# Kernel tuning notes

Measured on AMD Instinct MI355X. Metric: run time of the kernel, lower is better.

The kernel has to match this reference:

```python
import jax, jax.numpy as jnp
import numpy as np

N, E, F_IN, H, NSE, L, C, G = 50000, 800000, 128, 128, 16, 3, 10, 256


def setup_inputs() -> dict:
    key = jax.random.key(0)
    ks = jax.random.split(key, 32)
    sc = 0.05
    inp = {
        "x": jax.random.normal(ks[0], (N, F_IN), jnp.float32),
        "s": jax.random.normal(ks[1], (N, NSE), jnp.float32),
        "edge_index": jax.random.randint(ks[2], (2, E), 0, N, jnp.int64),
        "batch": jnp.sort(jax.random.randint(ks[3], (N,), 0, G, jnp.int64)),
        # pre: Linear(F_IN, H); embedding_s: Linear(NSE, H)
        "pre_w": jax.random.normal(ks[4], (F_IN, H), jnp.float32) * sc,
        "pre_b": jnp.zeros((H,), jnp.float32),
        "emb_w": jax.random.normal(ks[5], (NSE, H), jnp.float32) * sc,
        "emb_b": jnp.zeros((H,), jnp.float32),
        # per-layer GIN MLP: Linear(2H,H) -> ReLU -> Linear(H,H)
        "gin_w1": jax.random.normal(ks[6], (L, 2 * H, H), jnp.float32) * sc,
        "gin_b1": jnp.zeros((L, H), jnp.float32),
        "gin_w2": jax.random.normal(ks[7], (L, H, H), jnp.float32) * sc,
        "gin_b2": jnp.zeros((L, H), jnp.float32),
        # per-layer GCNConv(H, H)
        "gcn_w": jax.random.normal(ks[8], (L, H, H), jnp.float32) * sc,
        "gcn_b": jnp.zeros((L, H), jnp.float32),
        "whp_w": jax.random.normal(ks[9], (2 * H, H), jnp.float32) * sc,
        "whp_b": jnp.zeros((H,), jnp.float32),
        "post_w": jax.random.normal(ks[10], (H, H), jnp.float32) * sc,
        "post_b": jnp.zeros((H,), jnp.float32),
        "ro_w": jax.random.normal(ks[11], (H, C), jnp.float32) * sc,
        "ro_b": jnp.zeros((C,), jnp.float32),
    }
    return inp


def reference(x, s, edge_index, batch, pre_w, pre_b, emb_w, emb_b,
              gin_w1, gin_b1, gin_w2, gin_b2, gcn_w, gcn_b,
              whp_w, whp_b, post_w, post_b, ro_w, ro_b):
    src, dst = edge_index[0], edge_index[1]
    x = x @ pre_w + pre_b                      # [N, H]
    s = s @ emb_w + emb_b                      # [N, H]
    # GCN symmetric norm with self-loops (deg includes the +1 self loop)
    deg = jax.ops.segment_sum(jnp.ones((E,), x.dtype), dst, num_segments=N) + 1.0
    dinv = jax.lax.rsqrt(deg)                  # [N]
    enorm = (dinv[src] * dinv[dst])[:, None]   # [E, 1]
    self_norm = (dinv * dinv)[:, None]         # [N, 1]
    for i in range(L):
        xc = jnp.concatenate([x, s], axis=-1)  # [N, 2H]
        # GINConv (eps=0): nn(x_i + sum_j x_j)
        agg = jax.ops.segment_sum(xc[src], dst, num_segments=N)
        h = xc + agg
        h = jax.nn.relu(h @ gin_w1[i] + gin_b1[i]) @ gin_w2[i] + gin_b2[i]
        x = jax.nn.relu(h)                     # dropout is identity in eval mode
        # GCNConv on s stream
        hs = s @ gcn_w[i]
        sagg = jax.ops.segment_sum(hs[src] * enorm, dst, num_segments=N)
        s = jnp.tanh(sagg + hs * self_norm + gcn_b[i])
    x = jnp.concatenate([x, s], axis=-1) @ whp_w + whp_b
    g = jax.ops.segment_sum(x, batch, num_segments=G)   # global_add_pool [G, H]
    g = jax.nn.relu(g @ post_w + post_b)
    return jax.nn.log_softmax(g @ ro_w + ro_b, axis=1)
```

## Files before the change

### kernel.cpp

```cpp
#include <hip/hip_runtime.h>
#include <math.h>

typedef __attribute__((ext_vector_type(8))) short short8;
typedef __attribute__((ext_vector_type(4))) float f32x4;
typedef unsigned int uint;
typedef unsigned short ushort;

#define HGRID(n, b) (((n) + (b) - 1) / (b))

__device__ __forceinline__ ushort f2bu(float f) {
    uint x = __builtin_bit_cast(uint, f);
    x = (x + 0x7fffu + ((x >> 16) & 1u)) >> 16;
    return (ushort)x;
}
__device__ __forceinline__ float blo(uint u) {
    return __builtin_bit_cast(float, u << 16);
}
__device__ __forceinline__ float bhi(uint u) {
    return __builtin_bit_cast(float, u & 0xffff0000u);
}
__device__ __forceinline__ uint packbf(float a, float b) {
    return (uint)f2bu(a) | ((uint)f2bu(b) << 16);
}

__device__ __forceinline__ void gload16(const void* g, void* l) {
    __builtin_amdgcn_global_load_lds(
        (const __attribute__((address_space(1))) void*)g,
        (__attribute__((address_space(3))) void*)l, 16, 0, 0);
}


__global__ void init_kernel(int* __restrict__ cnt, int* __restrict__ cur,
                            float* __restrict__ gbuf, int N, int GH) {
    int i = blockIdx.x * 256 + threadIdx.x;
    if (i < N) { cnt[i] = 0; cur[i] = 0; }
    if (i < GH) gbuf[i] = 0.f;
}


__global__ void count_kernel(const int* __restrict__ dst, int* __restrict__ cnt, int E) {
    int e = blockIdx.x * 256 + threadIdx.x;
    if (e < E) atomicAdd(&cnt[dst[e]], 1);
}

__global__ void scan_part(const int* __restrict__ cnt, int* __restrict__ bsum, int N) {
    __shared__ int sh[256];
    int b = blockIdx.x, t = threadIdx.x;
    int base = b * 1024 + t * 4;
    int tsum = 0;
    if (base + 3 < N) {
        int4 v = *(const int4*)(cnt + base);
        tsum = v.x + v.y + v.z + v.w;
    } else {
        #pragma unroll
        for (int k = 0; k < 4; ++k) if (base + k < N) tsum += cnt[base + k];
    }
    sh[t] = tsum;
    __syncthreads();
    for (int d = 128; d > 0; d >>= 1) {
        if (t < d) sh[t] += sh[t + d];
        __syncthreads();
    }
    if (t == 0) bsum[b] = sh[0];
}

__global__ void scan_fill(const int* __restrict__ cnt, const int* __restrict__ bsum,
                          int* __restrict__ offs, float* __restrict__ dinv,
                          int N, int E) {
    __shared__ int sh[256];
    __shared__ int sbase;
    int b = blockIdx.x, t = threadIdx.x;

    if (t < 64) {
        int s = 0;
        for (int i = t; i < b; i += 64) s += bsum[i];
        #pragma unroll
        for (int d = 32; d > 0; d >>= 1) s += __shfl_down(s, d, 64);
        if (t == 0) sbase = s;
    }

    int base = b * 1024 + t * 4;
    int c[4] = {0, 0, 0, 0};
    if (base + 3 < N) {
        int4 v = *(const int4*)(cnt + base);
        c[0] = v.x; c[1] = v.y; c[2] = v.z; c[3] = v.w;
    } else {
        #pragma unroll
        for (int k = 0; k < 4; ++k) if (base + k < N) c[k] = cnt[base + k];
    }
    int tsum = c[0] + c[1] + c[2] + c[3];
    sh[t] = tsum;
    __syncthreads();
    for (int d = 1; d < 256; d <<= 1) {
        int o = (t >= d) ? sh[t - d] : 0;
        __syncthreads();
        sh[t] += o;
        __syncthreads();
    }
    int run = sbase + sh[t] - tsum;
    #pragma unroll
    for (int k = 0; k < 4; ++k) {
        if (base + k < N) {
            offs[base + k] = run;
            dinv[base + k] = rsqrtf((float)c[k] + 1.0f);
            run += c[k];
        }
    }
    if (b == 0 && t == 0) offs[N] = E;
}

__global__ void fill_kernel(const int* __restrict__ src, const int* __restrict__ dst,
                            const int* __restrict__ offs, int* __restrict__ cur,
                            const float* __restrict__ dinv, int2* __restrict__ epack, int E) {
    int e = blockIdx.x * 256 + threadIdx.x;
    if (e < E) {
        int d = dst[e];
        int sv = src[e];
        int p = offs[d] + atomicAdd(&cur[d], 1);
        epack[p] = make_int2(sv * 64, __float_as_int(dinv[sv]));
    }
}


struct PrepArgs {
    const float *x, *s;
    const float *pre_w, *pre_b, *emb_w, *emb_b, *gin_w1, *gcn_w, *gin_w2, *whp_w;
    ushort *xs, *Wt_preemb, *Wt_dual, *Wt_gin2, *Wt_whp;
    float *bias_comb;
    int L, N;
};

__global__ void prep_kernel(PrepArgs a) {
    long idx = (long)blockIdx.x * 256 + threadIdx.x;
    long nconv = (long)a.N * 24;
    if (idx < nconv) {
        int n = (int)(idx / 24), ch = (int)(idx % 24);
        uint4 o = {0u, 0u, 0u, 0u};
        if (ch < 16) {
            const float4* px = (const float4*)(a.x + (long)n * 128 + ch * 8);
            float4 u = px[0], v = px[1];
            o.x = packbf(u.x, u.y); o.y = packbf(u.z, u.w);
            o.z = packbf(v.x, v.y); o.w = packbf(v.z, v.w);
        } else if (ch < 18) {
            const float4* ps = (const float4*)(a.s + (long)n * 16 + (ch - 16) * 8);
            float4 u = ps[0], v = ps[1];
            o.x = packbf(u.x, u.y); o.y = packbf(u.z, u.w);
            o.z = packbf(v.x, v.y); o.w = packbf(v.z, v.w);
        }
        *(uint4*)(a.xs + idx * 8) = o;
        return;
    }
    idx -= nconv;
    if (idx < 49152) {
        int c = (int)(idx / 192), k = (int)(idx % 192);
        float v = 0.f;
        if (c < 128) { if (k < 128) v = a.pre_w[(long)k * 128 + c]; }
        else if (k >= 128 && k < 144) v = a.emb_w[(long)(k - 128) * 128 + (c - 128)];
        a.Wt_preemb[idx] = f2bu(v);
        return;
    }
    idx -= 49152;
    if (idx < (long)a.L * 65536) {
        int i = (int)(idx / 65536);
        int r = (int)(idx % 65536);
        int c = r / 256, k = r % 256;
        float v = 0.f;
        if (c < 128) v = a.gin_w1[(long)i * 32768 + (long)k * 128 + c];
        else if (k >= 128) v = a.gcn_w[(long)i * 16384 + (long)(k - 128) * 128 + (c - 128)];
        a.Wt_dual[idx] = f2bu(v);
        return;
    }
    idx -= (long)a.L * 65536;
    if (idx < (long)a.L * 16384) {
        int i = (int)(idx / 16384);
        int r = (int)(idx % 16384);
        int c = r / 128, k = r % 128;
        a.Wt_gin2[idx] = f2bu(a.gin_w2[(long)i * 16384 + (long)k * 128 + c]);
        return;
    }
    idx -= (long)a.L * 16384;
    if (idx < 32768) {
        int c = (int)(idx / 256), k = (int)(idx % 256);
        a.Wt_whp[idx] = f2bu(a.whp_w[(long)k * 128 + c]);
        return;
    }
    idx -= 32768;
    if (idx < 256) a.bias_comb[idx] = (idx < 128) ? a.pre_b[idx] : a.emb_b[idx - 128];
}


template<int KPAD, int BN>
__global__ __launch_bounds__(512) void lin_mfma(
    const ushort* __restrict__ A, int a_stride,
    const ushort* __restrict__ Wt, const float* __restrict__ bias,
    ushort* __restrict__ out, int o_stride, int N, int act, int interleaved)
{
    constexpr int BK = 64;
    constexpr int NF = BN / 64;
    __shared__ __align__(16) ushort LA[128][BK];
    __shared__ __align__(16) ushort LB[BN][BK];

    const int tid  = threadIdx.x;
    const int l    = tid & 63;
    const int w    = tid >> 6;
    const int wr   = w >> 2;
    const int wc   = w & 3;
    const int row0 = blockIdx.x * 128;
    const int l15  = l & 15;
    const int lhi  = l >> 4;
    const int lrow = l >> 3;
    const int lslot = l & 7;

    f32x4 acc[4][NF];
    #pragma unroll
    for (int m = 0; m < 4; ++m)
        #pragma unroll
        for (int n = 0; n < NF; ++n) acc[m][n] = (f32x4){0.f, 0.f, 0.f, 0.f};

    for (int k0 = 0; k0 < KPAD; k0 += BK) {
        __syncthreads();
        #pragma unroll
        for (int i = 0; i < 2; ++i) {
            int ci = w * 2 + i;
            int r  = ci * 8 + lrow;
            int gr = row0 + r; if (gr > N - 1) gr = N - 1;
            gload16(A + (long)gr * a_stride + k0 + ((lslot ^ (r & 7)) * 8), &LA[ci * 8][0]);
        }
        #pragma unroll
        for (int i = 0; i < NF; ++i) {
            int ci = w * NF + i;
            int c  = ci * 8 + lrow;
            gload16(Wt + (long)c * KPAD + k0 + ((lslot ^ (c & 7)) * 8), &LB[ci * 8][0]);
        }
        __syncthreads();
        #pragma unroll
        for (int kk = 0; kk < BK; kk += 32) {
            int chb = (kk >> 3) + lhi;
            short8 a[4];
            #pragma unroll
            for (int m = 0; m < 4; ++m) {
                int r = wr * 64 + m * 16 + l15;
                a[m] = *(const short8*)&LA[r][(chb ^ (r & 7)) * 8];
            }
            #pragma unroll
            for (int n = 0; n < NF; ++n) {
                int c = wc * (BN / 4) + n * 16 + l15;
                short8 b = *(const short8*)&LB[c][(chb ^ (c & 7)) * 8];
                #pragma unroll
                for (int m = 0; m < 4; ++m)
                    acc[m][n] = __builtin_amdgcn_mfma_f32_16x16x32_bf16(a[m], b, acc[m][n], 0, 0, 0);
            }
        }
    }

    #pragma unroll
    for (int n = 0; n < NF; ++n) {
        int col = wc * (BN / 4) + n * 16 + l15;
        float bv = bias ? bias[col] : 0.f;
        #pragma unroll
        for (int m = 0; m < 4; ++m) {
            #pragma unroll
            for (int j = 0; j < 4; ++j) {
                int gr = row0 + wr * 64 + m * 16 + (lhi << 2) + j;
                if (gr < N) {
                    float v = acc[m][n][j] + bv;
                    if (act) v = fmaxf(v, 0.f);
                    long off;
                    if (interleaved) {
                        int cc = col & 127;
                        off = (long)gr * 256 + 4 * (cc >> 1) + ((col >> 7) << 1) + (cc & 1);
                    } else {
                        off = (long)gr * o_stride + col;
                    }
                    out[off] = f2bu(v);
                }
            }
        }
    }
}


__global__ __launch_bounds__(256) void fused_gather(
    const uint2* __restrict__ yh, const int* __restrict__ offs,
    const int2* __restrict__ epack,
    const float* __restrict__ dinv,
    const float* __restrict__ b1, const float* __restrict__ gb,
    uint* __restrict__ h1p, uint* __restrict__ xcp, int N)
{
    int node = blockIdx.x * 4 + (threadIdx.x >> 6);
    if (node >= N) return;
    int l = threadIdx.x & 63;

    uint2 self = yh[(long)node * 64 + l];
    float di = dinv[node];
    float g0 = blo(self.x), g1 = bhi(self.x);
    float s0 = 0.f, s1 = 0.f;

    int j0 = offs[node], j1 = offs[node + 1];
    int jmid = j0 + ((j1 - j0) & ~7);

    for (int j = j0; j < jmid; j += 8) {
        int2 e[8]; uint2 v[8];
        #pragma unroll
        for (int k = 0; k < 8; ++k) e[k] = epack[j + k];
        #pragma unroll
        for (int k = 0; k < 8; ++k) v[k] = yh[e[k].x + l];
        #pragma unroll
        for (int k = 0; k < 8; ++k) {
            float ds = __int_as_float(e[k].y);
            g0 += blo(v[k].x);
            g1 += bhi(v[k].x);
            s0 += blo(v[k].y) * ds;
            s1 += bhi(v[k].y) * ds;
        }
    }
    if (jmid < j1) {
        int2 e[8]; uint2 v[8];
        #pragma unroll
        for (int k = 0; k < 8; ++k) {
            int jj = jmid + k;
            e[k] = epack[(jj < j1) ? jj : (j1 - 1)];
            if (jj >= j1) e[k].y = 0;
        }
        #pragma unroll
        for (int k = 0; k < 8; ++k) v[k] = yh[e[k].x + l];
        #pragma unroll
        for (int k = 0; k < 8; ++k) {
            float ds = __int_as_float(e[k].y);
            float m = (jmid + k < j1) ? 1.f : 0.f;
            g0 += blo(v[k].x) * m;
            g1 += bhi(v[k].x) * m;
            s0 += blo(v[k].y) * ds;
            s1 += bhi(v[k].y) * ds;
        }
    }

    float2 bb = ((const float2*)b1)[l];
    g0 = fmaxf(g0 + bb.x, 0.f);
    g1 = fmaxf(g1 + bb.y, 0.f);
    h1p[(long)node * 64 + l] = packbf(g0, g1);

    float dii = di * di;
    float2 gg = ((const float2*)gb)[l];
    float t0 = tanhf(s0 * di + blo(self.y) * dii + gg.x);
    float t1 = tanhf(s1 * di + bhi(self.y) * dii + gg.y);
    xcp[(long)node * 128 + 64 + l] = packbf(t0, t1);
}


__global__ void pool_kernel(const ushort* __restrict__ xh, const int* __restrict__ batch,
                            float* __restrict__ g, int N) {
    int c  = threadIdx.x;
    int n0 = blockIdx.x * 128;
    if (n0 >= N) return;
    int n1 = min(n0 + 128, N);
    int curg = batch[n0];
    float acc = 0.f;
    for (int n = n0; n < n1; ++n) {
        int b = batch[n];
        if (b != curg) {
            atomicAdd(&g[(long)curg * 128 + c], acc);
            acc = 0.f;
            curg = b;
        }
        acc += blo((uint)xh[(long)n * 128 + c]);
    }
    atomicAdd(&g[(long)curg * 128 + c], acc);
}


__global__ void head_kernel(const float* __restrict__ g, const float* __restrict__ post_w,
                            const float* __restrict__ post_b, const float* __restrict__ ro_w,
                            const float* __restrict__ ro_b, float* __restrict__ out, int C) {
    __shared__ float row[128];
    __shared__ float g2[128];
    __shared__ float lg[16];
    __shared__ float s_lse;
    int gi = blockIdx.x;
    int c  = threadIdx.x;
    row[c] = g[(long)gi * 128 + c];
    __syncthreads();
    float acc = post_b[c];
    for (int k = 0; k < 128; ++k) acc += row[k] * post_w[k * 128 + c];
    g2[c] = fmaxf(acc, 0.f);
    __syncthreads();
    if (c < C) {
        float a = ro_b[c];
        for (int k = 0; k < 128; ++k) a += g2[k] * ro_w[k * C + c];
        lg[c] = a;
    }
    __syncthreads();
    if (c == 0) {
        float m = lg[0];
        for (int i = 1; i < C; ++i) m = fmaxf(m, lg[i]);
        float sum = 0.f;
        for (int i = 0; i < C; ++i) sum += expf(lg[i] - m);
        s_lse = m + logf(sum);
    }
    __syncthreads();
    if (c < C) out[(long)gi * C + c] = lg[c] - s_lse;
}


extern "C" void kernel_launch(void* const* d_in, const int* in_sizes, int n_in,
                              void* d_out, int out_size, void* d_ws, size_t ws_size,
                              hipStream_t stream) {
    const float* x      = (const float*)d_in[0];
    const float* s_in   = (const float*)d_in[1];
    const int*   ei     = (const int*)d_in[2];
    const int*   batch  = (const int*)d_in[3];
    const float* pre_w  = (const float*)d_in[4];
    const float* pre_b  = (const float*)d_in[5];
    const float* emb_w  = (const float*)d_in[6];
    const float* emb_b  = (const float*)d_in[7];
    const float* gin_w1 = (const float*)d_in[8];
    const float* gin_b1 = (const float*)d_in[9];
    const float* gin_w2 = (const float*)d_in[10];
    const float* gin_b2 = (const float*)d_in[11];
    const float* gcn_w  = (const float*)d_in[12];
    const float* gcn_b  = (const float*)d_in[13];
    const float* whp_w  = (const float*)d_in[14];
    const float* whp_b  = (const float*)d_in[15];
    const float* post_w = (const float*)d_in[16];
    const float* post_b = (const float*)d_in[17];
    const float* ro_w   = (const float*)d_in[18];
    const float* ro_b   = (const float*)d_in[19];

    const int H = 128;
    const int N = in_sizes[0] / 128;
    const int E = in_sizes[2] / 2;
    const int C = in_sizes[19];
    const int G = out_size / C;
    const int L = in_sizes[9] / H;

    const int* srcv = ei;
    const int* dstv = ei + E;

    char* p = (char*)d_ws;
    auto alloc = [&](size_t bytes) -> void* {
        void* r = (void*)p;
        p += (bytes + 255) & ~(size_t)255;
        return r;
    };
    ushort* xc   = (ushort*)alloc((size_t)N * 256 * 2);
    ushort* yh   = (ushort*)alloc((size_t)N * 256 * 2);
    ushort* h1   = (ushort*)alloc((size_t)N * 128 * 2);
    ushort* xs   = (ushort*)alloc((size_t)N * 192 * 2);
    ushort* ybuf = (ushort*)alloc((size_t)N * 128 * 2);
    ushort* Wt_preemb = (ushort*)alloc(256 * 192 * 2);
    ushort* Wt_dual   = (ushort*)alloc((size_t)L * 256 * 256 * 2);
    ushort* Wt_gin2   = (ushort*)alloc((size_t)L * 128 * 128 * 2);
    ushort* Wt_whp    = (ushort*)alloc(128 * 256 * 2);
    float*  bias_comb = (float*)alloc(256 * 4);
    float*  dinv = (float*)alloc((size_t)N * 4);
    float*  gbuf = (float*)alloc((size_t)G * 128 * 4);
    int* cnt   = (int*)alloc((size_t)N * 4);
    int* offs  = (int*)alloc((size_t)(N + 1) * 4);
    int* cur   = (int*)alloc((size_t)N * 4);
    int* bsum  = (int*)alloc((size_t)HGRID(N, 1024) * 4);
    int2* epack = (int2*)alloc((size_t)E * 8);

    const int nb = HGRID(N, 1024);

    init_kernel<<<HGRID(N, 256), 256, 0, stream>>>(cnt, cur, gbuf, N, G * 128);
    count_kernel<<<HGRID(E, 256), 256, 0, stream>>>(dstv, cnt, E);
    scan_part<<<nb, 256, 0, stream>>>(cnt, bsum, N);
    scan_fill<<<nb, 256, 0, stream>>>(cnt, bsum, offs, dinv, N, E);
    fill_kernel<<<HGRID(E, 256), 256, 0, stream>>>(srcv, dstv, offs, cur, dinv, epack, E);

    PrepArgs pa;
    pa.x = x; pa.s = s_in;
    pa.pre_w = pre_w; pa.pre_b = pre_b; pa.emb_w = emb_w; pa.emb_b = emb_b;
    pa.gin_w1 = gin_w1; pa.gcn_w = gcn_w; pa.gin_w2 = gin_w2; pa.whp_w = whp_w;
    pa.xs = xs; pa.Wt_preemb = Wt_preemb; pa.Wt_dual = Wt_dual; pa.Wt_gin2 = Wt_gin2;
    pa.Wt_whp = Wt_whp; pa.bias_comb = bias_comb; pa.L = L; pa.N = N;
    long prep_tot = (long)N * 24 + 49152 + (long)L * 65536 + (long)L * 16384 + 32768 + 256;
    prep_kernel<<<HGRID(prep_tot, 256), 256, 0, stream>>>(pa);

    const int lb = HGRID(N, 128);
    lin_mfma<192, 256><<<lb, 512, 0, stream>>>(xs, 192, Wt_preemb, bias_comb,
                                               xc, 256, N, 0, 0);

    for (int i = 0; i < L; ++i) {
        lin_mfma<256, 256><<<lb, 512, 0, stream>>>(xc, 256, Wt_dual + (size_t)i * 65536,
                                                   nullptr, yh, 256, N, 0, 1);
        fused_gather<<<HGRID(N, 4), 256, 0, stream>>>(
            (const uint2*)yh, offs, epack, dinv,
            gin_b1 + (size_t)i * H, gcn_b + (size_t)i * H,
            (uint*)h1, (uint*)xc, N);
        lin_mfma<128, 128><<<lb, 512, 0, stream>>>(h1, 128, Wt_gin2 + (size_t)i * 16384,
                                                   gin_b2 + (size_t)i * H, xc, 256, N, 1, 0);
    }

    lin_mfma<256, 128><<<lb, 512, 0, stream>>>(xc, 256, Wt_whp, whp_b, ybuf, 128, N, 0, 0);

    pool_kernel<<<HGRID(N, 128), 128, 0, stream>>>(ybuf, batch, gbuf, N);
    head_kernel<<<G, 128, 0, stream>>>(gbuf, post_w, post_b, ro_w, ro_b, (float*)d_out, C);
}
```

Baseline: 447.2 us.

## Split gather feature dimension into eight column slices across blocks

```diff
diff --git a/kernel.cpp b/kernel.cpp
--- a/kernel.cpp
+++ b/kernel.cpp
@@ -287,47 +287,33 @@
     const float* __restrict__ b1, const float* __restrict__ gb,
     uint* __restrict__ h1p, uint* __restrict__ xcp, int N)
 {
-    int node = blockIdx.x * 4 + (threadIdx.x >> 6);
+    int sb    = blockIdx.x;
+    int slice = sb & 7;
+    int node  = (sb >> 3) * 32 + (threadIdx.x >> 3);
     if (node >= N) return;
-    int l = threadIdx.x & 63;
-
-    uint2 self = yh[(long)node * 64 + l];
+    int lg = threadIdx.x & 7;
+    int w  = slice * 8 + lg;
+
+    uint2 self = yh[(long)node * 64 + w];
     float di = dinv[node];
     float g0 = blo(self.x), g1 = bhi(self.x);
     float s0 = 0.f, s1 = 0.f;
 
     int j0 = offs[node], j1 = offs[node + 1];
-    int jmid = j0 + ((j1 - j0) & ~7);
-
-    for (int j = j0; j < jmid; j += 8) {
-        int2 e[8]; uint2 v[8];
-        #pragma unroll
-        for (int k = 0; k < 8; ++k) e[k] = epack[j + k];
-        #pragma unroll
-        for (int k = 0; k < 8; ++k) v[k] = yh[e[k].x + l];
-        #pragma unroll
-        for (int k = 0; k < 8; ++k) {
-            float ds = __int_as_float(e[k].y);
-            g0 += blo(v[k].x);
-            g1 += bhi(v[k].x);
-            s0 += blo(v[k].y) * ds;
-            s1 += bhi(v[k].y) * ds;
-        }
-    }
-    if (jmid < j1) {
-        int2 e[8]; uint2 v[8];
-        #pragma unroll
-        for (int k = 0; k < 8; ++k) {
-            int jj = jmid + k;
+    for (int j = j0; j < j1; j += 4) {
+        int2 e[4]; uint2 v[4];
+        #pragma unroll
+        for (int k = 0; k < 4; ++k) {
+            int jj = j + k;
             e[k] = epack[(jj < j1) ? jj : (j1 - 1)];
             if (jj >= j1) e[k].y = 0;
         }
         #pragma unroll
-        for (int k = 0; k < 8; ++k) v[k] = yh[e[k].x + l];
-        #pragma unroll
-        for (int k = 0; k < 8; ++k) {
+        for (int k = 0; k < 4; ++k) v[k] = yh[e[k].x + w];
+        #pragma unroll
+        for (int k = 0; k < 4; ++k) {
             float ds = __int_as_float(e[k].y);
-            float m = (jmid + k < j1) ? 1.f : 0.f;
+            float m = (j + k < j1) ? 1.f : 0.f;
             g0 += blo(v[k].x) * m;
             g1 += bhi(v[k].x) * m;
             s0 += blo(v[k].y) * ds;
@@ -335,16 +321,16 @@
         }
     }
 
-    float2 bb = ((const float2*)b1)[l];
+    float2 bb = ((const float2*)b1)[w];
     g0 = fmaxf(g0 + bb.x, 0.f);
     g1 = fmaxf(g1 + bb.y, 0.f);
-    h1p[(long)node * 64 + l] = packbf(g0, g1);
+    h1p[(long)node * 64 + w] = packbf(g0, g1);
 
     float dii = di * di;
-    float2 gg = ((const float2*)gb)[l];
+    float2 gg = ((const float2*)gb)[w];
     float t0 = tanhf(s0 * di + blo(self.y) * dii + gg.x);
     float t1 = tanhf(s1 * di + bhi(self.y) * dii + gg.y);
-    xcp[(long)node * 128 + 64 + l] = packbf(t0, t1);
+    xcp[(long)node * 128 + 64 + w] = packbf(t0, t1);
 }
 
 
@@ -481,10 +467,11 @@
     lin_mfma<192, 256><<<lb, 512, 0, stream>>>(xs, 192, Wt_preemb, bias_comb,
                                                xc, 256, N, 0, 0);
 
+    const int gb_blocks = HGRID(N, 32) * 8;
     for (int i = 0; i < L; ++i) {
         lin_mfma<256, 256><<<lb, 512, 0, stream>>>(xc, 256, Wt_dual + (size_t)i * 65536,
                                                    nullptr, yh, 256, N, 0, 1);
-        fused_gather<<<HGRID(N, 4), 256, 0, stream>>>(
+        fused_gather<<<gb_blocks, 256, 0, stream>>>(
             (const uint2*)yh, offs, epack, dinv,
             gin_b1 + (size_t)i * H, gcn_b + (size_t)i * H,
             (uint*)h1, (uint*)xc, N);
```

Measured after the change: 532.8 us. +19.1%, slower.
